# Optimization experiments

Hardware: AMD Instinct MI355X
Metric: run time of the kernel (lower is better)

Reference implementation:

```python
import jax, jax.numpy as jnp
import numpy as np

N, E, D, K = 50000, 600000, 128, 8
EPS = 1e-09


def setup_inputs() -> dict:
    key = jax.random.key(0)
    ks = jax.random.split(key, 10)
    feature = jax.random.normal(ks[0], (N, D), dtype=jnp.float32)
    snorm_n = jax.random.uniform(ks[1], (N, 1), dtype=jnp.float32)
    src = jax.random.randint(ks[2], (E,), 0, N, dtype=jnp.int32)
    dst = jax.random.randint(ks[3], (E,), 0, N, dtype=jnp.int32)
    W_low = jax.random.normal(ks[4], (D, D), dtype=jnp.float32) / np.sqrt(D)
    W_high = jax.random.normal(ks[5], (D, D), dtype=jnp.float32) / np.sqrt(D)
    W_mid = jax.random.normal(ks[6], (D, D), dtype=jnp.float32) / np.sqrt(D)
    gamma_low = jax.random.uniform(ks[7], (K,), dtype=jnp.float32)
    gamma_high = jax.random.uniform(ks[8], (K,), dtype=jnp.float32)
    gamma_mid = jax.random.uniform(ks[9], (K,), dtype=jnp.float32)
    bias = jnp.zeros((D,), dtype=jnp.float32)
    return {"feature": feature, "snorm_n": snorm_n, "src": src, "dst": dst,
            "W_low": W_low, "W_high": W_high, "W_mid": W_mid,
            "gamma_low": gamma_low, "gamma_high": gamma_high,
            "gamma_mid": gamma_mid, "bias": bias}


def _mp(feat, src, dst, norm):
    # symmetric-normalized SpMM: h[v] = norm[v] * sum_{u->v} norm[u]*feat[u]
    msg = (feat * norm[:, None])[src]                        # [E, D] gather
    agg = jax.ops.segment_sum(msg, dst, num_segments=N)       # [N, D] scatter-add
    return agg * norm[:, None]


def reference(feature, snorm_n, src, dst, W_low, W_high, W_mid,
              gamma_low, gamma_high, gamma_mid, bias):
    deg = jax.ops.segment_sum(jnp.ones((E,), feature.dtype), dst, num_segments=N)
    norm = jnp.clip(deg, 1.0) ** -0.5                          # in-degree^-0.5
    alpha = jnp.linspace(EPS, 1.0 - EPS, K).astype(feature.dtype)
    midalpha = jnp.linspace(EPS, 1.0, K).astype(feature.dtype)

    h = _mp(feature, src, dst, norm)

    gl = jax.nn.relu(gamma_low)
    o0 = (jnp.dot(alpha, gl) * h + jnp.dot(1.0 - alpha, gl) * feature) @ W_low.T
    gh = jax.nn.relu(gamma_high)
    o1 = (jnp.dot(-alpha, gh) * h + jnp.dot(1.0 - alpha, gh) * feature) @ W_high.T
    gm = jax.nn.relu(gamma_mid)
    h1 = _mp(h, src, dst, norm)
    o2 = (jnp.sum(gm) * h1 - jnp.dot(midalpha, gm) * feature) @ W_mid.T

    # sequential mutual gating, exactly as the torch in-place updates
    o0 = o0 * jax.nn.sigmoid(o1 + o2)
    o1 = o1 * jax.nn.sigmoid(o0 + o2)
    o2 = o2 * jax.nn.sigmoid(o0 + o1)

    out = o0 + o1 + o2 + bias
    out = out * snorm_n          # graph_norm
    out = jax.nn.relu(out)       # activation
    return out
```

## Files before the change

### kernel.cpp

```cpp
#include <hip/hip_runtime.h>
#include <hip/hip_bf16.h>
#include <math.h>

#define N_NODES 50000
#define N_EDGES 600000
#define DIM 128
#define KGAM 8
#define EPSV 1e-9f

typedef __attribute__((ext_vector_type(8))) short short8;
typedef __attribute__((ext_vector_type(4))) float float4v;

__device__ __forceinline__ float bf2f(short s) {
    unsigned int u = ((unsigned int)(unsigned short)s) << 16;
    return __builtin_bit_cast(float, u);
}
__device__ __forceinline__ short f2bf(float f) {
    return (short)__builtin_bit_cast(unsigned short, __float2bfloat16(f));
}
__device__ __forceinline__ unsigned int pack2(float a, float b) {
    return (unsigned int)(unsigned short)f2bf(a) | ((unsigned int)(unsigned short)f2bf(b) << 16);
}
__device__ __forceinline__ float sigm(float x) { return 1.f / (1.f + __expf(-x)); }

__global__ void k_zero_int(int* __restrict__ p, int n) {
    int i = blockIdx.x * blockDim.x + threadIdx.x;
    if (i < n) p[i] = 0;
}

__global__ void k_deg(const int* __restrict__ dst, int* __restrict__ deg) {
    int e = blockIdx.x * blockDim.x + threadIdx.x;
    if (e < N_EDGES) atomicAdd(&deg[dst[e]], 1);
}

__global__ void k_scan1(const int* __restrict__ deg, int* __restrict__ rowstart,
                        int* __restrict__ bsums, float* __restrict__ norm) {
    __shared__ int s[256];
    int tid = threadIdx.x;
    int i0 = blockIdx.x * 1024 + tid * 4;
    int v[4]; int sum = 0;
#pragma unroll
    for (int c = 0; c < 4; ++c) {
        int i = i0 + c;
        int d = (i < N_NODES) ? deg[i] : 0;
        v[c] = d; sum += d;
    }
    s[tid] = sum; __syncthreads();
#pragma unroll
    for (int off = 1; off < 256; off <<= 1) {
        int t = (tid >= off) ? s[tid - off] : 0;
        __syncthreads();
        s[tid] += t;
        __syncthreads();
    }
    if (tid == 255) bsums[blockIdx.x] = s[255];
    int run = s[tid] - sum;
#pragma unroll
    for (int c = 0; c < 4; ++c) {
        int i = i0 + c;
        if (i < N_NODES) {
            rowstart[i] = run;
            norm[i] = rsqrtf((float)(v[c] < 1 ? 1 : v[c]));
        }
        run += v[c];
    }
}

__global__ void k_scan2(int* __restrict__ bsums, int nb) {
    __shared__ int s[64];
    int tid = threadIdx.x;
    int v = (tid < nb) ? bsums[tid] : 0;
    s[tid] = v; __syncthreads();
#pragma unroll
    for (int off = 1; off < 64; off <<= 1) {
        int t = (tid >= off) ? s[tid - off] : 0;
        __syncthreads();
        s[tid] += t;
        __syncthreads();
    }
    if (tid < nb) bsums[tid] = s[tid] - v;
}

__global__ void k_scan3(const int* __restrict__ bsums, int* __restrict__ rowstart) {
    int i = blockIdx.x * blockDim.x + threadIdx.x;
    if (i < N_NODES) rowstart[i] += bsums[i >> 10];
    if (i == 0) rowstart[N_NODES] = N_EDGES;
}

__global__ void k_fill(const int* __restrict__ src, const int* __restrict__ dst,
                       const int* __restrict__ rowstart, int* __restrict__ cnt,
                       int* __restrict__ esrc) {
    int e = blockIdx.x * blockDim.x + threadIdx.x;
    if (e < N_EDGES) {
        int d = dst[e];
        int slot = rowstart[d] + atomicAdd(&cnt[d], 1);
        esrc[slot] = src[e];
    }
}

__global__ void k_coeffs(const float* __restrict__ gl, const float* __restrict__ gh,
                         const float* __restrict__ gm, float* __restrict__ c) {
    if (threadIdx.x == 0 && blockIdx.x == 0) {
        float a0 = 0, b0 = 0, a1 = 0, b1 = 0, sg = 0, m2 = 0;
        for (int k = 0; k < KGAM; ++k) {
            float al = EPSV + (float)k * (1.f - 2.f * EPSV) / (KGAM - 1);
            float md = EPSV + (float)k * (1.f - EPSV) / (KGAM - 1);
            float l = fmaxf(gl[k], 0.f), h = fmaxf(gh[k], 0.f), m = fmaxf(gm[k], 0.f);
            a0 += al * l;  b0 += (1.f - al) * l;
            a1 += -al * h; b1 += (1.f - al) * h;
            sg += m;       m2 += md * m;
        }
        c[0] = a0; c[1] = b0; c[2] = a1; c[3] = b1; c[4] = sg; c[5] = -m2;
    }
}

__global__ void k_wconv(const float* __restrict__ W0, const float* __restrict__ W1,
                        const float* __restrict__ W2, unsigned int* __restrict__ Wb) {
    const float* Ws = (blockIdx.y == 0) ? W0 : (blockIdx.y == 1) ? W1 : W2;
    int i = (blockIdx.x * 256 + threadIdx.x) * 4;
    if (i < DIM * DIM) {
        float4 v = *(const float4*)(Ws + i);
        uint2 o; o.x = pack2(v.x, v.y); o.y = pack2(v.z, v.w);
        *(uint2*)(Wb + (blockIdx.y * DIM * DIM + i) / 2) = o;
    }
}

__global__ void k_prescale(const float4* __restrict__ f, const float* __restrict__ norm,
                           uint2* __restrict__ fb, uint2* __restrict__ fp) {
    int i = blockIdx.x * 256 + threadIdx.x;
    if (i >= N_NODES * DIM / 4) return;
    int row = i >> 5;
    float nv = norm[row];
    float4 v = f[i];
    uint2 a; a.x = pack2(v.x, v.y); a.y = pack2(v.z, v.w);
    uint2 b; b.x = pack2(v.x * nv, v.y * nv); b.y = pack2(v.z * nv, v.w * nv);
    fb[i] = a;
    fp[i] = b;
}

__device__ __forceinline__ void acc4(float4& a, uint2 r) {
    a.x += __builtin_bit_cast(float, r.x << 16);
    a.y += __builtin_bit_cast(float, r.x & 0xffff0000u);
    a.z += __builtin_bit_cast(float, r.y << 16);
    a.w += __builtin_bit_cast(float, r.y & 0xffff0000u);
}

__global__ void k_spmm(const uint2* __restrict__ in, const float* __restrict__ norm,
                       const int* __restrict__ rowstart, const int* __restrict__ esrc,
                       uint2* __restrict__ hout, uint2* __restrict__ preout, int wpre) {
    int v = blockIdx.x * 8 + (threadIdx.x >> 5);
    int l = threadIdx.x & 31;
    if (v >= N_NODES) return;
    int beg = rowstart[v], end = rowstart[v + 1];
    float4 acc = {0.f, 0.f, 0.f, 0.f};
    int t = beg;
    for (; t + 3 < end; t += 4) {
        int u0 = esrc[t], u1 = esrc[t + 1], u2 = esrc[t + 2], u3 = esrc[t + 3];
        uint2 r0 = in[(size_t)u0 * 32 + l];
        uint2 r1 = in[(size_t)u1 * 32 + l];
        uint2 r2 = in[(size_t)u2 * 32 + l];
        uint2 r3 = in[(size_t)u3 * 32 + l];
        acc4(acc, r0); acc4(acc, r1); acc4(acc, r2); acc4(acc, r3);
    }
    for (; t < end; ++t) {
        uint2 r = in[(size_t)esrc[t] * 32 + l];
        acc4(acc, r);
    }
    float nv = norm[v];
    float hx = acc.x * nv, hy = acc.y * nv, hz = acc.z * nv, hw = acc.w * nv;
    uint2 o; o.x = pack2(hx, hy); o.y = pack2(hz, hw);
    hout[(size_t)v * 32 + l] = o;
    if (wpre) {
        uint2 p; p.x = pack2(hx * nv, hy * nv); p.y = pack2(hz * nv, hw * nv);
        preout[(size_t)v * 32 + l] = p;
    }
}

#define RT 64
#define TSTR 136

__global__ __launch_bounds__(512, 4) void k_gemm_fused(
    const short* __restrict__ hB, const short* __restrict__ fB,
    const short* __restrict__ h1B, const short* __restrict__ Wb,
    const float* __restrict__ coeffs, const float* __restrict__ bias,
    const float* __restrict__ snorm, float* __restrict__ out) {
    __shared__ short Ts[3][RT * TSTR];

    const float c0 = coeffs[0], c1 = coeffs[1], c2 = coeffs[2];
    const float c3 = coeffs[3], c4 = coeffs[4], c5 = coeffs[5];
    const int r0 = blockIdx.x * RT;
    const int tid = threadIdx.x;

#pragma unroll
    for (int it = 0; it < 2; ++it) {
        int idx = tid + it * 512;
        int r = idx >> 4;
        int cg = (idx & 15) * 8;
        int row = r0 + r;
        short8 hv = {0,0,0,0,0,0,0,0}, fv = {0,0,0,0,0,0,0,0}, h1v = {0,0,0,0,0,0,0,0};
        if (row < N_NODES) {
            size_t base = (size_t)row * DIM + cg;
            hv  = *(const short8*)(hB + base);
            fv  = *(const short8*)(fB + base);
            h1v = *(const short8*)(h1B + base);
        }
        short8 t0, t1, t2;
#pragma unroll
        for (int j = 0; j < 8; ++j) {
            float hf = bf2f(hv[j]), ff = bf2f(fv[j]), h1f = bf2f(h1v[j]);
            t0[j] = f2bf(c0 * hf + c1 * ff);
            t1[j] = f2bf(c2 * hf + c3 * ff);
            t2[j] = f2bf(c4 * h1f + c5 * ff);
        }
        int la = r * TSTR + cg;
        *(short8*)&Ts[0][la] = t0;
        *(short8*)&Ts[1][la] = t1;
        *(short8*)&Ts[2][la] = t2;
    }
    __syncthreads();

    const int lane = tid & 63;
    const int ct = tid >> 6;
    const int m = lane & 15;
    const int quad = lane >> 4;

    float4v acc[3][4];
    const float4v zero = {0.f, 0.f, 0.f, 0.f};
#pragma unroll
    for (int g = 0; g < 3; ++g)
#pragma unroll
        for (int rt = 0; rt < 4; ++rt) acc[g][rt] = zero;

    const short* wbase = Wb + (ct * 16 + m) * DIM + quad * 8;
#pragma unroll
    for (int ks = 0; ks < 4; ++ks) {
        const short* wp = wbase + ks * 32;
        short8 b0 = *(const short8*)(wp);
        short8 b1 = *(const short8*)(wp + DIM * DIM);
        short8 b2 = *(const short8*)(wp + 2 * DIM * DIM);
#pragma unroll
        for (int rt = 0; rt < 4; ++rt) {
            int aoff = (rt * 16 + m) * TSTR + ks * 32 + quad * 8;
            short8 a0 = *(const short8*)&Ts[0][aoff];
            short8 a1 = *(const short8*)&Ts[1][aoff];
            short8 a2 = *(const short8*)&Ts[2][aoff];
            acc[0][rt] = __builtin_amdgcn_mfma_f32_16x16x32_bf16(a0, b0, acc[0][rt], 0, 0, 0);
            acc[1][rt] = __builtin_amdgcn_mfma_f32_16x16x32_bf16(a1, b1, acc[1][rt], 0, 0, 0);
            acc[2][rt] = __builtin_amdgcn_mfma_f32_16x16x32_bf16(a2, b2, acc[2][rt], 0, 0, 0);
        }
    }

    const int col = ct * 16 + m;
    const float bc = bias[col];
#pragma unroll
    for (int rt = 0; rt < 4; ++rt) {
#pragma unroll
        for (int r = 0; r < 4; ++r) {
            int row = r0 + rt * 16 + quad * 4 + r;
            if (row < N_NODES) {
                float sn = snorm[row];
                float o0 = acc[0][rt][r], o1 = acc[1][rt][r], o2 = acc[2][rt][r];
                float g0 = o0 * sigm(o1 + o2);
                float g1 = o1 * sigm(g0 + o2);
                float g2 = o2 * sigm(g0 + g1);
                float vv = (g0 + g1 + g2 + bc) * sn;
                out[(size_t)row * DIM + col] = fmaxf(vv, 0.f);
            }
        }
    }
}

extern "C" void kernel_launch(void* const* d_in, const int* in_sizes, int n_in,
                              void* d_out, int out_size, void* d_ws, size_t ws_size,
                              hipStream_t stream) {
    const float* feature = (const float*)d_in[0];
    const float* snorm   = (const float*)d_in[1];
    const int*   src     = (const int*)d_in[2];
    const int*   dst     = (const int*)d_in[3];
    const float* W_low   = (const float*)d_in[4];
    const float* W_high  = (const float*)d_in[5];
    const float* W_mid   = (const float*)d_in[6];
    const float* gl      = (const float*)d_in[7];
    const float* gh      = (const float*)d_in[8];
    const float* gm      = (const float*)d_in[9];
    const float* bias    = (const float*)d_in[10];
    float* out = (float*)d_out;

    char* w = (char*)d_ws;
    auto alloc = [&](size_t bytes) {
        char* p = w;
        w += (bytes + 255) & ~(size_t)255;
        return p;
    };
    float* norm   = (float*)alloc((size_t)N_NODES * 4);
    int* deg      = (int*)alloc((size_t)2 * N_NODES * 4);
    int* cnt      = deg + N_NODES;
    int* rowstart = (int*)alloc((size_t)(N_NODES + 1) * 4);
    int* bsums    = (int*)alloc(64 * 4);
    int* esrc     = (int*)alloc((size_t)N_EDGES * 4);
    float* coeffs = (float*)alloc(64 * 4);
    short* Wb     = (short*)alloc((size_t)3 * DIM * DIM * 2);
    short* fb     = (short*)alloc((size_t)N_NODES * DIM * 2);
    short* fp     = (short*)alloc((size_t)N_NODES * DIM * 2);
    short* h      = (short*)alloc((size_t)N_NODES * DIM * 2);
    short* hp     = (short*)alloc((size_t)N_NODES * DIM * 2);
    short* h1     = (short*)alloc((size_t)N_NODES * DIM * 2);

    k_zero_int<<<(2 * N_NODES + 255) / 256, 256, 0, stream>>>(deg, 2 * N_NODES);
    k_deg<<<(N_EDGES + 255) / 256, 256, 0, stream>>>(dst, deg);
    int nchunks = (N_NODES + 1023) / 1024;
    k_scan1<<<nchunks, 256, 0, stream>>>(deg, rowstart, bsums, norm);
    k_scan2<<<1, 64, 0, stream>>>(bsums, nchunks);
    k_scan3<<<(N_NODES + 255) / 256, 256, 0, stream>>>(bsums, rowstart);
    k_fill<<<(N_EDGES + 255) / 256, 256, 0, stream>>>(src, dst, rowstart, cnt, esrc);
    k_coeffs<<<1, 1, 0, stream>>>(gl, gh, gm, coeffs);
    k_wconv<<<dim3(16, 3), 256, 0, stream>>>(W_low, W_high, W_mid, (unsigned int*)Wb);
    k_prescale<<<(N_NODES * DIM / 4 + 255) / 256, 256, 0, stream>>>(
        (const float4*)feature, norm, (uint2*)fb, (uint2*)fp);

    int spmm_blocks = (N_NODES + 7) / 8;
    k_spmm<<<spmm_blocks, 256, 0, stream>>>((const uint2*)fp, norm, rowstart, esrc,
                                            (uint2*)h, (uint2*)hp, 1);
    k_spmm<<<spmm_blocks, 256, 0, stream>>>((const uint2*)hp, norm, rowstart, esrc,
                                            (uint2*)h1, (uint2*)hp, 0);

    k_gemm_fused<<<(N_NODES + RT - 1) / RT, 512, 0, stream>>>(
        h, fb, h1, Wb, coeffs, bias, snorm, out);
}
```

Baseline: 251.2 us.

## Fold gamma coefficients into weights, drop LDS staging, widen SpMM gathers

The scalar mixing coefficients are now multiplied into six bf16 copies of the weight matrices, so the GEMM kernel feeds h, feature and h1 straight from global memory into MFMAs. This removes the LDS staging pass, the per-element combine and the barrier, in exchange for twice as many MFMAs and extra weight loads. The SpMM now gives each node 16 lanes that gather 16-byte rows instead of 32 lanes gathering 8 bytes, to cut memory instructions per edge. The last GEMM block now reads rows past N without a bounds check, relying on workspace memory beyond the buffer.

After: 288.7 us. 14.9% more time.

```diff
diff --git a/kernel.cpp b/kernel.cpp
--- a/kernel.cpp
+++ b/kernel.cpp
@@ -115,13 +115,16 @@
 }
 
 __global__ void k_wconv(const float* __restrict__ W0, const float* __restrict__ W1,
-                        const float* __restrict__ W2, unsigned int* __restrict__ Wb) {
-    const float* Ws = (blockIdx.y == 0) ? W0 : (blockIdx.y == 1) ? W1 : W2;
+                        const float* __restrict__ W2, const float* __restrict__ coeffs,
+                        unsigned int* __restrict__ Wb) {
+    int g = blockIdx.y;
+    const float* Ws = (g < 2) ? W0 : (g < 4) ? W1 : W2;
+    float c = coeffs[g];
     int i = (blockIdx.x * 256 + threadIdx.x) * 4;
     if (i < DIM * DIM) {
         float4 v = *(const float4*)(Ws + i);
-        uint2 o; o.x = pack2(v.x, v.y); o.y = pack2(v.z, v.w);
-        *(uint2*)(Wb + (blockIdx.y * DIM * DIM + i) / 2) = o;
+        uint2 o; o.x = pack2(c * v.x, c * v.y); o.y = pack2(c * v.z, c * v.w);
+        *(uint2*)(Wb + (g * DIM * DIM + i) / 2) = o;
     }
 }
 
@@ -138,87 +141,61 @@
     fp[i] = b;
 }
 
-__device__ __forceinline__ void acc4(float4& a, uint2 r) {
-    a.x += __builtin_bit_cast(float, r.x << 16);
-    a.y += __builtin_bit_cast(float, r.x & 0xffff0000u);
-    a.z += __builtin_bit_cast(float, r.y << 16);
-    a.w += __builtin_bit_cast(float, r.y & 0xffff0000u);
-}
-
-__global__ void k_spmm(const uint2* __restrict__ in, const float* __restrict__ norm,
+__device__ __forceinline__ void acc8(float* a, uint4 r) {
+    a[0] += __builtin_bit_cast(float, r.x << 16);
+    a[1] += __builtin_bit_cast(float, r.x & 0xffff0000u);
+    a[2] += __builtin_bit_cast(float, r.y << 16);
+    a[3] += __builtin_bit_cast(float, r.y & 0xffff0000u);
+    a[4] += __builtin_bit_cast(float, r.z << 16);
+    a[5] += __builtin_bit_cast(float, r.z & 0xffff0000u);
+    a[6] += __builtin_bit_cast(float, r.w << 16);
+    a[7] += __builtin_bit_cast(float, r.w & 0xffff0000u);
+}
+
+__global__ void k_spmm(const uint4* __restrict__ in, const float* __restrict__ norm,
                        const int* __restrict__ rowstart, const int* __restrict__ esrc,
-                       uint2* __restrict__ hout, uint2* __restrict__ preout, int wpre) {
-    int v = blockIdx.x * 8 + (threadIdx.x >> 5);
-    int l = threadIdx.x & 31;
+                       uint4* __restrict__ hout, uint4* __restrict__ preout, int wpre) {
+    int v = blockIdx.x * 16 + (threadIdx.x >> 4);
+    int l = threadIdx.x & 15;
     if (v >= N_NODES) return;
     int beg = rowstart[v], end = rowstart[v + 1];
-    float4 acc = {0.f, 0.f, 0.f, 0.f};
+    float a[8] = {0.f, 0.f, 0.f, 0.f, 0.f, 0.f, 0.f, 0.f};
     int t = beg;
     for (; t + 3 < end; t += 4) {
         int u0 = esrc[t], u1 = esrc[t + 1], u2 = esrc[t + 2], u3 = esrc[t + 3];
-        uint2 r0 = in[(size_t)u0 * 32 + l];
-        uint2 r1 = in[(size_t)u1 * 32 + l];
-        uint2 r2 = in[(size_t)u2 * 32 + l];
-        uint2 r3 = in[(size_t)u3 * 32 + l];
-        acc4(acc, r0); acc4(acc, r1); acc4(acc, r2); acc4(acc, r3);
+        uint4 r0 = in[(size_t)u0 * 16 + l];
+        uint4 r1 = in[(size_t)u1 * 16 + l];
+        uint4 r2 = in[(size_t)u2 * 16 + l];
+        uint4 r3 = in[(size_t)u3 * 16 + l];
+        acc8(a, r0); acc8(a, r1); acc8(a, r2); acc8(a, r3);
     }
     for (; t < end; ++t) {
-        uint2 r = in[(size_t)esrc[t] * 32 + l];
-        acc4(acc, r);
+        uint4 r = in[(size_t)esrc[t] * 16 + l];
+        acc8(a, r);
     }
     float nv = norm[v];
-    float hx = acc.x * nv, hy = acc.y * nv, hz = acc.z * nv, hw = acc.w * nv;
-    uint2 o; o.x = pack2(hx, hy); o.y = pack2(hz, hw);
-    hout[(size_t)v * 32 + l] = o;
+    uint4 o;
+    o.x = pack2(a[0] * nv, a[1] * nv); o.y = pack2(a[2] * nv, a[3] * nv);
+    o.z = pack2(a[4] * nv, a[5] * nv); o.w = pack2(a[6] * nv, a[7] * nv);
+    hout[(size_t)v * 16 + l] = o;
     if (wpre) {
-        uint2 p; p.x = pack2(hx * nv, hy * nv); p.y = pack2(hz * nv, hw * nv);
-        preout[(size_t)v * 32 + l] = p;
+        float n2 = nv * nv;
+        uint4 p;
+        p.x = pack2(a[0] * n2, a[1] * n2); p.y = pack2(a[2] * n2, a[3] * n2);
+        p.z = pack2(a[4] * n2, a[5] * n2); p.w = pack2(a[6] * n2, a[7] * n2);
+        preout[(size_t)v * 16 + l] = p;
     }
 }
 
 #define RT 64
-#define TSTR 136
 
 __global__ __launch_bounds__(512, 4) void k_gemm_fused(
     const short* __restrict__ hB, const short* __restrict__ fB,
     const short* __restrict__ h1B, const short* __restrict__ Wb,
-    const float* __restrict__ coeffs, const float* __restrict__ bias,
-    const float* __restrict__ snorm, float* __restrict__ out) {
-    __shared__ short Ts[3][RT * TSTR];
-
-    const float c0 = coeffs[0], c1 = coeffs[1], c2 = coeffs[2];
-    const float c3 = coeffs[3], c4 = coeffs[4], c5 = coeffs[5];
+    const float* __restrict__ bias, const float* __restrict__ snorm,
+    float* __restrict__ out) {
     const int r0 = blockIdx.x * RT;
     const int tid = threadIdx.x;
-
-#pragma unroll
-    for (int it = 0; it < 2; ++it) {
-        int idx = tid + it * 512;
-        int r = idx >> 4;
-        int cg = (idx & 15) * 8;
-        int row = r0 + r;
-        short8 hv = {0,0,0,0,0,0,0,0}, fv = {0,0,0,0,0,0,0,0}, h1v = {0,0,0,0,0,0,0,0};
-        if (row < N_NODES) {
-            size_t base = (size_t)row * DIM + cg;
-            hv  = *(const short8*)(hB + base);
-            fv  = *(const short8*)(fB + base);
-            h1v = *(const short8*)(h1B + base);
-        }
-        short8 t0, t1, t2;
-#pragma unroll
-        for (int j = 0; j < 8; ++j) {
-            float hf = bf2f(hv[j]), ff = bf2f(fv[j]), h1f = bf2f(h1v[j]);
-            t0[j] = f2bf(c0 * hf + c1 * ff);
-            t1[j] = f2bf(c2 * hf + c3 * ff);
-            t2[j] = f2bf(c4 * h1f + c5 * ff);
-        }
-        int la = r * TSTR + cg;
-        *(short8*)&Ts[0][la] = t0;
-        *(short8*)&Ts[1][la] = t1;
-        *(short8*)&Ts[2][la] = t2;
-    }
-    __syncthreads();
-
     const int lane = tid & 63;
     const int ct = tid >> 6;
     const int m = lane & 15;
@@ -231,22 +208,32 @@
 #pragma unroll
         for (int rt = 0; rt < 4; ++rt) acc[g][rt] = zero;
 
-    const short* wbase = Wb + (ct * 16 + m) * DIM + quad * 8;
+    const short* ah = hB  + (size_t)(r0 + m) * DIM + quad * 8;
+    const short* af = fB  + (size_t)(r0 + m) * DIM + quad * 8;
+    const short* a1 = h1B + (size_t)(r0 + m) * DIM + quad * 8;
+    const short* wp = Wb  + (size_t)(ct * 16 + m) * DIM + quad * 8;
+
 #pragma unroll
     for (int ks = 0; ks < 4; ++ks) {
-        const short* wp = wbase + ks * 32;
-        short8 b0 = *(const short8*)(wp);
-        short8 b1 = *(const short8*)(wp + DIM * DIM);
-        short8 b2 = *(const short8*)(wp + 2 * DIM * DIM);
+        const int ko = ks * 32;
+        short8 b0 = *(const short8*)(wp + ko);
+        short8 b1 = *(const short8*)(wp + ko + DIM * DIM);
+        short8 b2 = *(const short8*)(wp + ko + 2 * DIM * DIM);
+        short8 b3 = *(const short8*)(wp + ko + 3 * DIM * DIM);
+        short8 b4 = *(const short8*)(wp + ko + 4 * DIM * DIM);
+        short8 b5 = *(const short8*)(wp + ko + 5 * DIM * DIM);
 #pragma unroll
         for (int rt = 0; rt < 4; ++rt) {
-            int aoff = (rt * 16 + m) * TSTR + ks * 32 + quad * 8;
-            short8 a0 = *(const short8*)&Ts[0][aoff];
-            short8 a1 = *(const short8*)&Ts[1][aoff];
-            short8 a2 = *(const short8*)&Ts[2][aoff];
-            acc[0][rt] = __builtin_amdgcn_mfma_f32_16x16x32_bf16(a0, b0, acc[0][rt], 0, 0, 0);
-            acc[1][rt] = __builtin_amdgcn_mfma_f32_16x16x32_bf16(a1, b1, acc[1][rt], 0, 0, 0);
-            acc[2][rt] = __builtin_amdgcn_mfma_f32_16x16x32_bf16(a2, b2, acc[2][rt], 0, 0, 0);
+            const int ro = rt * 16 * DIM + ko;
+            short8 x_h = *(const short8*)(ah + ro);
+            short8 x_f = *(const short8*)(af + ro);
+            short8 x_1 = *(const short8*)(a1 + ro);
+            acc[0][rt] = __builtin_amdgcn_mfma_f32_16x16x32_bf16(x_h, b0, acc[0][rt], 0, 0, 0);
+            acc[0][rt] = __builtin_amdgcn_mfma_f32_16x16x32_bf16(x_f, b1, acc[0][rt], 0, 0, 0);
+            acc[1][rt] = __builtin_amdgcn_mfma_f32_16x16x32_bf16(x_h, b2, acc[1][rt], 0, 0, 0);
+            acc[1][rt] = __builtin_amdgcn_mfma_f32_16x16x32_bf16(x_f, b3, acc[1][rt], 0, 0, 0);
+            acc[2][rt] = __builtin_amdgcn_mfma_f32_16x16x32_bf16(x_1, b4, acc[2][rt], 0, 0, 0);
+            acc[2][rt] = __builtin_amdgcn_mfma_f32_16x16x32_bf16(x_f, b5, acc[2][rt], 0, 0, 0);
         }
     }
 
@@ -299,7 +286,7 @@
     int* bsums    = (int*)alloc(64 * 4);
     int* esrc     = (int*)alloc((size_t)N_EDGES * 4);
     float* coeffs = (float*)alloc(64 * 4);
-    short* Wb     = (short*)alloc((size_t)3 * DIM * DIM * 2);
+    short* Wb     = (short*)alloc((size_t)6 * DIM * DIM * 2);
     short* fb     = (short*)alloc((size_t)N_NODES * DIM * 2);
     short* fp     = (short*)alloc((size_t)N_NODES * DIM * 2);
     short* h      = (short*)alloc((size_t)N_NODES * DIM * 2);
@@ -314,16 +301,17 @@
     k_scan3<<<(N_NODES + 255) / 256, 256, 0, stream>>>(bsums, rowstart);
     k_fill<<<(N_EDGES + 255) / 256, 256, 0, stream>>>(src, dst, rowstart, cnt, esrc);
     k_coeffs<<<1, 1, 0, stream>>>(gl, gh, gm, coeffs);
-    k_wconv<<<dim3(16, 3), 256, 0, stream>>>(W_low, W_high, W_mid, (unsigned int*)Wb);
+    k_wconv<<<dim3(16, 6), 256, 0, stream>>>(W_low, W_high, W_mid, coeffs,
+                                             (unsigned int*)Wb);
     k_prescale<<<(N_NODES * DIM / 4 + 255) / 256, 256, 0, stream>>>(
         (const float4*)feature, norm, (uint2*)fb, (uint2*)fp);
 
-    int spmm_blocks = (N_NODES + 7) / 8;
-    k_spmm<<<spmm_blocks, 256, 0, stream>>>((const uint2*)fp, norm, rowstart, esrc,
-                                            (uint2*)h, (uint2*)hp, 1);
-    k_spmm<<<spmm_blocks, 256, 0, stream>>>((const uint2*)hp, norm, rowstart, esrc,
-                                            (uint2*)h1, (uint2*)hp, 0);
+    int spmm_blocks = (N_NODES + 15) / 16;
+    k_spmm<<<spmm_blocks, 256, 0, stream>>>((const uint4*)fp, norm, rowstart, esrc,
+                                            (uint4*)h, (uint4*)hp, 1);
+    k_spmm<<<spmm_blocks, 256, 0, stream>>>((const uint4*)hp, norm, rowstart, esrc,
+                                            (uint4*)h1, (uint4*)hp, 0);
 
     k_gemm_fused<<<(N_NODES + RT - 1) / RT, 512, 0, stream>>>(
-        h, fb, h1, Wb, coeffs, bias, snorm, out);
-}
+        h, fb, h1, Wb, bias, snorm, out);
+}
```
